# Kernel optimization log

Measured on AMD Instinct MI355X. Metric: run time of the kernel, lower is better.

Reference implementation:

```python
import jax, jax.numpy as jnp
import numpy as np

G, B, T, D, U = 3, 32, 1024, 512, 512  # branches, batch, time, feat dim, units

def setup_inputs() -> dict:
    key = jax.random.key(0)
    ks = jax.random.split(key, 8)
    s = 0.02
    return {
        "query": jax.random.normal(ks[0], (G, B, D), jnp.float32),
        "values": jax.random.normal(ks[1], (G, B, T, D), jnp.float32),
        "W1": jax.random.normal(ks[2], (G, D, U), jnp.float32) * s,
        "b1": jnp.zeros((G, U), jnp.float32),
        "W2": jax.random.normal(ks[3], (G, D, U), jnp.float32) * s,
        "b2": jnp.zeros((G, U), jnp.float32),
        "V": jax.random.normal(ks[4], (G, U), jnp.float32) * s,
        "bV": jnp.zeros((G,), jnp.float32),
    }

def reference(query, values, W1, b1, W2, b2, V, bV):
    # query: [G,B,D], values: [G,B,T,D]; G=3 independent additive-attention branches.
    qp = jnp.einsum('gbd,gdu->gbu', query, W1) + b1[:, None, :]          # [G,B,U]
    vp = jnp.einsum('gbtd,gdu->gbtu', values, W2) + b2[:, None, None, :]  # [G,B,T,U]
    feat = jnp.tanh(qp[:, :, None, :] + vp)                               # [G,B,T,U]
    score = jnp.einsum('gbtu,gu->gbt', feat, V) + bV[:, None, None]       # [G,B,T]
    weights = jax.nn.softmax(score, axis=2)                               # softmax over time
    context = jnp.einsum('gbt,gbtd->gbd', weights, values)                # [G,B,D]
    return context, weights[..., None]  # matches tf.stack outputs: [3,B,D], [3,B,T,1]
```

## Files before the change

### kernel.cpp

```cpp
#include <hip/hip_runtime.h>
#include <cstdint>
#include <cstddef>

#define NG 3
#define NB 32
#define NT 1024
#define ND 512
#define NU 512

typedef __bf16 bf16x8 __attribute__((ext_vector_type(8)));
typedef float  f32x16 __attribute__((ext_vector_type(16)));

static __device__ __forceinline__ unsigned int f2bf(float f) {
    union { float f; unsigned int u; } v; v.f = f;
    return (v.u + 0x7FFFu + ((v.u >> 16) & 1u)) >> 16;
}

static __device__ __forceinline__ bf16x8 ld_bf16x8(const char* base, int off) {
    return __builtin_bit_cast(bf16x8, *(const uint4*)(base + off));
}

__global__ __launch_bounds__(256) void prep_qb_kernel(
    const float* __restrict__ query, const float* __restrict__ W1,
    const float* __restrict__ b1, const float* __restrict__ b2,
    float* __restrict__ qb)
{
    __shared__ float qs[NB][ND];
    const int g  = blockIdx.x >> 3;
    const int uc = blockIdx.x & 7;
    const int tid = threadIdx.x;

    const float4* qsrc = (const float4*)(query + (size_t)g * NB * ND);
    #pragma unroll
    for (int i = 0; i < 16; ++i)
        ((float4*)&qs[0][0])[tid + i * 256] = qsrc[tid + i * 256];
    __syncthreads();

    const int u  = uc * 64 + (tid & 63);
    const int b0 = tid >> 6;
    float acc[8] = {};
    const float* w1col = W1 + (size_t)g * ND * NU + u;
    for (int d = 0; d < ND; ++d) {
        float w = w1col[(size_t)d * NU];
        #pragma unroll
        for (int j = 0; j < 8; ++j)
            acc[j] = fmaf(qs[b0 + 4 * j][d], w, acc[j]);
    }
    const float bias = b1[g * NU + u] + b2[g * NU + u];
    #pragma unroll
    for (int j = 0; j < 8; ++j)
        qb[((size_t)g * NB + (b0 + 4 * j)) * NU + u] = acc[j] + bias;
}

__global__ __launch_bounds__(256) void prep_w2t_kernel(
    const float* __restrict__ W2, char* __restrict__ w2t)
{
    __shared__ float tile[64][65];
    const int g  = blockIdx.x >> 6;
    const int tb = blockIdx.x & 63;
    const int d0 = (tb >> 3) * 64;
    const int u0 = (tb & 7) * 64;
    const int tx = threadIdx.x & 63;
    const int ty = threadIdx.x >> 6;

    const float* src = W2 + (size_t)g * ND * NU;
    #pragma unroll
    for (int k = 0; k < 16; ++k) {
        int r = ty + 4 * k;
        tile[r][tx] = src[(size_t)(d0 + r) * NU + (u0 + tx)];
    }
    __syncthreads();
    char* dstg = w2t + (size_t)g * 16 * 32768;
    #pragma unroll
    for (int k = 0; k < 16; ++k) {
        int ul = ty + 4 * k;
        int u  = u0 + ul;
        int d  = d0 + tx;
        unsigned short h = (unsigned short)f2bf(tile[tx][ul]);
        int r = u & 31;
        size_t off = (size_t)(u >> 5) * 32768
                   + (size_t)(((r << 10) | (d << 1)) ^ ((r & 7) << 4));
        *(unsigned short*)(dstg + off) = h;
    }
}

__global__ __launch_bounds__(256, 2) void score_kernel(
    const float* __restrict__ values, const char* __restrict__ w2t,
    const float* __restrict__ qb, const float* __restrict__ Vvec,
    const float* __restrict__ bV, float* __restrict__ scores)
{
    __shared__ char  Bs[2][32768];
    __shared__ float qbs[NU];
    __shared__ float Vs[NU];

    const int blk = blockIdx.x;
    const int g   = blk >> 8;
    const int rem = blk & 255;
    const int b   = rem >> 3;
    const int t0  = (rem & 7) << 7;
    const int tid  = threadIdx.x;
    const int lane = tid & 63;
    const int wave = tid >> 6;

    const char* w2g = w2t + ((size_t)g << 19);

    {
        const char* src = w2g + (wave << 13) + (lane << 4);
        char* dst = &Bs[0][wave << 13];
        #pragma unroll
        for (int i = 0; i < 8; ++i)
            __builtin_amdgcn_global_load_lds(
                (const __attribute__((address_space(1))) void*)(src + (i << 10)),
                (__attribute__((address_space(3))) void*)(dst + (i << 10)),
                16, 0, 0);
    }

    bf16x8 afrag[32];
    {
        const int arow_t = t0 + (wave << 5) + (lane & 31);
        const float* arow = values + (((size_t)g * NB + b) * NT + arow_t) * ND;
        const int acol = (lane >> 5) << 3;
        #pragma unroll
        for (int kk = 0; kk < 32; ++kk) {
            const float4* ap = (const float4*)(arow + (kk << 4) + acol);
            float4 v0 = ap[0], v1 = ap[1];
            union { bf16x8 v; unsigned int u[4]; } t;
            t.u[0] = f2bf(v0.x) | (f2bf(v0.y) << 16);
            t.u[1] = f2bf(v0.z) | (f2bf(v0.w) << 16);
            t.u[2] = f2bf(v1.x) | (f2bf(v1.y) << 16);
            t.u[3] = f2bf(v1.z) | (f2bf(v1.w) << 16);
            afrag[kk] = t.v;
        }
    }

    {
        const float* qsrc = qb + ((size_t)g * NB + b) * NU;
        qbs[tid]       = qsrc[tid];
        qbs[tid + 256] = qsrc[tid + 256];
        Vs[tid]        = Vvec[g * NU + tid];
        Vs[tid + 256]  = Vvec[g * NU + tid + 256];
    }

    asm volatile("s_waitcnt vmcnt(0) lgkmcnt(0)" ::: "memory");
    __builtin_amdgcn_s_barrier();

    const int brow  = lane & 31;
    const int bbase = (brow << 10) + ((lane >> 5) << 4);
    const int bswz  = (lane & 7) << 4;

    float p[16] = {};

    #pragma unroll 1
    for (int uc = 0; uc < 16; ++uc) {
        if (uc < 15) {
            const char* src = w2g + (((size_t)(uc + 1)) << 15) + (wave << 13) + (lane << 4);
            char* dst = &Bs[(uc + 1) & 1][wave << 13];
            #pragma unroll
            for (int i = 0; i < 8; ++i)
                __builtin_amdgcn_global_load_lds(
                    (const __attribute__((address_space(1))) void*)(src + (i << 10)),
                    (__attribute__((address_space(3))) void*)(dst + (i << 10)),
                    16, 0, 0);
        }

        const char* bsL = Bs[uc & 1];
        f32x16 acc = (f32x16)(0.0f);
        #pragma unroll
        for (int kk = 0; kk < 32; ++kk) {
            bf16x8 bfv = ld_bf16x8(bsL, (bbase + (kk << 5)) ^ bswz);
            acc = __builtin_amdgcn_mfma_f32_32x32x16_bf16(afrag[kk], bfv, acc, 0, 0, 0);
        }

        const int u = (uc << 5) + brow;
        const float qv = qbs[u], vv = Vs[u];
        #pragma unroll
        for (int r = 0; r < 16; ++r) {
            float x  = acc[r] + qv;
            float e  = __expf(-2.f * fabsf(x));
            float th = (1.f - e) / (1.f + e);
            th = copysignf(th, x);
            p[r] = fmaf(th, vv, p[r]);
        }

        asm volatile("s_waitcnt vmcnt(0)" ::: "memory");
        __builtin_amdgcn_s_barrier();
    }

    #pragma unroll
    for (int r = 0; r < 16; ++r) {
        float v = p[r];
        v += __shfl_xor(v, 1);
        v += __shfl_xor(v, 2);
        v += __shfl_xor(v, 4);
        v += __shfl_xor(v, 8);
        v += __shfl_xor(v, 16);
        p[r] = v;
    }
    if ((lane & 31) == 0) {
        const float bv = bV[g];
        float* srow = scores + ((size_t)g * NB + b) * NT + t0 + (wave << 5);
        #pragma unroll
        for (int r = 0; r < 16; ++r) {
            int t_local = (r & 3) + 8 * (r >> 2) + 4 * (lane >> 5);
            srow[t_local] = p[r] + bv;
        }
    }
}

__global__ __launch_bounds__(256) void finish_kernel(
    const float* __restrict__ scores, const float* __restrict__ values,
    float* __restrict__ out_ctx, float* __restrict__ out_w)
{
    __shared__ float sl[NT];
    __shared__ float red[16];
    const int gb  = blockIdx.x;
    const int tid = threadIdx.x;
    const int lane = tid & 63, wid = tid >> 6;

    const float* srow = scores + (size_t)gb * NT;
    float s[4];
    #pragma unroll
    for (int j = 0; j < 4; ++j) s[j] = srow[tid + 256 * j];

    float m = fmaxf(fmaxf(s[0], s[1]), fmaxf(s[2], s[3]));
    #pragma unroll
    for (int mask = 32; mask; mask >>= 1) m = fmaxf(m, __shfl_xor(m, mask));
    if (lane == 0) red[wid] = m;
    __syncthreads();
    const float gm = fmaxf(fmaxf(red[0], red[1]), fmaxf(red[2], red[3]));

    float e[4], ps = 0.f;
    #pragma unroll
    for (int j = 0; j < 4; ++j) { e[j] = __expf(s[j] - gm); ps += e[j]; }
    #pragma unroll
    for (int mask = 32; mask; mask >>= 1) ps += __shfl_xor(ps, mask);
    if (lane == 0) red[8 + wid] = ps;
    __syncthreads();
    const float inv = 1.f / (red[8] + red[9] + red[10] + red[11]);

    #pragma unroll
    for (int j = 0; j < 4; ++j) {
        float w = e[j] * inv;
        sl[tid + 256 * j] = w;
        out_w[(size_t)gb * NT + tid + 256 * j] = w;
    }
    __syncthreads();

    const float* vbase = values + (size_t)gb * NT * ND + 2 * tid;
    float2 a0 = {0.f, 0.f}, a1 = {0.f, 0.f}, a2 = {0.f, 0.f}, a3 = {0.f, 0.f};
    #pragma unroll 2
    for (int t = 0; t < NT; t += 4) {
        float2 v0 = *(const float2*)(vbase + (size_t)(t + 0) * ND);
        float2 v1 = *(const float2*)(vbase + (size_t)(t + 1) * ND);
        float2 v2 = *(const float2*)(vbase + (size_t)(t + 2) * ND);
        float2 v3 = *(const float2*)(vbase + (size_t)(t + 3) * ND);
        float w0 = sl[t], w1 = sl[t + 1], w2 = sl[t + 2], w3 = sl[t + 3];
        a0.x = fmaf(w0, v0.x, a0.x); a0.y = fmaf(w0, v0.y, a0.y);
        a1.x = fmaf(w1, v1.x, a1.x); a1.y = fmaf(w1, v1.y, a1.y);
        a2.x = fmaf(w2, v2.x, a2.x); a2.y = fmaf(w2, v2.y, a2.y);
        a3.x = fmaf(w3, v3.x, a3.x); a3.y = fmaf(w3, v3.y, a3.y);
    }
    float2 r;
    r.x = (a0.x + a1.x) + (a2.x + a3.x);
    r.y = (a0.y + a1.y) + (a2.y + a3.y);
    *(float2*)(out_ctx + (size_t)gb * ND + 2 * tid) = r;
}

extern "C" void kernel_launch(void* const* d_in, const int* in_sizes, int n_in,
                              void* d_out, int out_size, void* d_ws, size_t ws_size,
                              hipStream_t stream)
{
    (void)in_sizes; (void)n_in; (void)out_size; (void)ws_size;
    const float* query  = (const float*)d_in[0];
    const float* values = (const float*)d_in[1];
    const float* W1     = (const float*)d_in[2];
    const float* b1     = (const float*)d_in[3];
    const float* W2     = (const float*)d_in[4];
    const float* b2     = (const float*)d_in[5];
    const float* Vv     = (const float*)d_in[6];
    const float* bV     = (const float*)d_in[7];

    float* out_ctx = (float*)d_out;
    float* out_w   = out_ctx + (size_t)NG * NB * ND;

    float* qb     = (float*)d_ws;
    float* scores = qb + (size_t)NG * NB * NU;
    char*  w2t    = (char*)(scores + (size_t)NG * NB * NT);

    prep_qb_kernel <<<NG * 8,             256, 0, stream>>>(query, W1, b1, b2, qb);
    prep_w2t_kernel<<<NG * 64,            256, 0, stream>>>(W2, w2t);
    score_kernel   <<<NG * NB * (NT/128), 256, 0, stream>>>(values, w2t, qb, Vv, bV, scores);
    finish_kernel  <<<NG * NB,            256, 0, stream>>>(scores, values, out_ctx, out_w);
}
```

Baseline: 181.5 us.

## Triple-buffer W2 in half-K stages and split finish kernel across D slices

```diff
diff --git a/kernel.cpp b/kernel.cpp
--- a/kernel.cpp
+++ b/kernel.cpp
@@ -84,12 +84,12 @@
     }
 }
 
-__global__ __launch_bounds__(256, 2) void score_kernel(
+__global__ __launch_bounds__(256, 3) void score_kernel(
     const float* __restrict__ values, const char* __restrict__ w2t,
     const float* __restrict__ qb, const float* __restrict__ Vvec,
     const float* __restrict__ bV, float* __restrict__ scores)
 {
-    __shared__ char  Bs[2][32768];
+    __shared__ char  Bs[3][16384];
     __shared__ float qbs[NU];
     __shared__ float Vs[NU];
 
@@ -104,16 +104,20 @@
 
     const char* w2g = w2t + ((size_t)g << 19);
 
-    {
-        const char* src = w2g + (wave << 13) + (lane << 4);
-        char* dst = &Bs[0][wave << 13];
-        #pragma unroll
-        for (int i = 0; i < 8; ++i)
+    auto stage = [&](int ph) {
+        const char* src = w2g + ((size_t)(ph >> 1) << 15) + ((ph & 1) << 9)
+                        + (wave << 13) + ((lane >> 5) << 10) + ((lane & 31) << 4);
+        char* dst = &Bs[ph % 3][(wave << 12) + (lane << 4)];
+        #pragma unroll
+        for (int i = 0; i < 4; ++i)
             __builtin_amdgcn_global_load_lds(
-                (const __attribute__((address_space(1))) void*)(src + (i << 10)),
+                (const __attribute__((address_space(1))) void*)(src + (i << 11)),
                 (__attribute__((address_space(3))) void*)(dst + (i << 10)),
                 16, 0, 0);
-    }
+    };
+
+    stage(0);
+    stage(1);
 
     bf16x8 afrag[32];
     {
@@ -141,49 +145,52 @@
         Vs[tid + 256]  = Vvec[g * NU + tid + 256];
     }
 
-    asm volatile("s_waitcnt vmcnt(0) lgkmcnt(0)" ::: "memory");
+    asm volatile("s_waitcnt vmcnt(4) lgkmcnt(0)" ::: "memory");
     __builtin_amdgcn_s_barrier();
 
     const int brow  = lane & 31;
-    const int bbase = (brow << 10) + ((lane >> 5) << 4);
-    const int bswz  = (lane & 7) << 4;
+    const int bswz  = (brow & 7) << 4;
+    const int bbase = (brow << 9) + ((lane >> 5) << 4);
 
     float p[16] = {};
+    f32x16 acc = (f32x16)(0.0f);
 
     #pragma unroll 1
-    for (int uc = 0; uc < 16; ++uc) {
-        if (uc < 15) {
-            const char* src = w2g + (((size_t)(uc + 1)) << 15) + (wave << 13) + (lane << 4);
-            char* dst = &Bs[(uc + 1) & 1][wave << 13];
+    for (int ph = 0; ph < 32; ++ph) {
+        if (ph < 30) stage(ph + 2);
+
+        const char* bsL = Bs[ph % 3];
+        if ((ph & 1) == 0) acc = (f32x16)(0.0f);
+
+        __builtin_amdgcn_s_setprio(1);
+        #pragma unroll
+        for (int kk = 0; kk < 16; ++kk) {
+            bf16x8 bfv = ld_bf16x8(bsL, (bbase + (kk << 5)) ^ bswz);
+            acc = __builtin_amdgcn_mfma_f32_32x32x16_bf16(
+                      afrag[((ph & 1) << 4) + kk], bfv, acc, 0, 0, 0);
+        }
+        __builtin_amdgcn_s_setprio(0);
+
+        if (ph & 1) {
+            const int u = ((ph >> 1) << 5) + brow;
+            const float qv = qbs[u], vv = Vs[u];
             #pragma unroll
-            for (int i = 0; i < 8; ++i)
-                __builtin_amdgcn_global_load_lds(
-                    (const __attribute__((address_space(1))) void*)(src + (i << 10)),
-                    (__attribute__((address_space(3))) void*)(dst + (i << 10)),
-                    16, 0, 0);
-        }
-
-        const char* bsL = Bs[uc & 1];
-        f32x16 acc = (f32x16)(0.0f);
-        #pragma unroll
-        for (int kk = 0; kk < 32; ++kk) {
-            bf16x8 bfv = ld_bf16x8(bsL, (bbase + (kk << 5)) ^ bswz);
-            acc = __builtin_amdgcn_mfma_f32_32x32x16_bf16(afrag[kk], bfv, acc, 0, 0, 0);
-        }
-
-        const int u = (uc << 5) + brow;
-        const float qv = qbs[u], vv = Vs[u];
-        #pragma unroll
-        for (int r = 0; r < 16; ++r) {
-            float x  = acc[r] + qv;
-            float e  = __expf(-2.f * fabsf(x));
-            float th = (1.f - e) / (1.f + e);
-            th = copysignf(th, x);
-            p[r] = fmaf(th, vv, p[r]);
-        }
-
-        asm volatile("s_waitcnt vmcnt(0)" ::: "memory");
-        __builtin_amdgcn_s_barrier();
+            for (int r = 0; r < 16; ++r) {
+                float x  = acc[r] + qv;
+                float e  = __expf(-2.f * fabsf(x));
+                float th = (1.f - e) / (1.f + e);
+                th = copysignf(th, x);
+                p[r] = fmaf(th, vv, p[r]);
+            }
+        }
+
+        if (ph < 30) {
+            asm volatile("s_waitcnt vmcnt(4)" ::: "memory");
+            __builtin_amdgcn_s_barrier();
+        } else if (ph == 30) {
+            asm volatile("s_waitcnt vmcnt(0)" ::: "memory");
+            __builtin_amdgcn_s_barrier();
+        }
     }
 
     #pragma unroll
@@ -213,7 +220,10 @@
 {
     __shared__ float sl[NT];
     __shared__ float red[16];
-    const int gb  = blockIdx.x;
+    __shared__ float cred[4][128];
+    const int blk   = blockIdx.x;
+    const int gb    = blk >> 2;
+    const int slice = blk & 3;
     const int tid = threadIdx.x;
     const int lane = tid & 63, wid = tid >> 6;
 
@@ -242,28 +252,28 @@
     for (int j = 0; j < 4; ++j) {
         float w = e[j] * inv;
         sl[tid + 256 * j] = w;
-        out_w[(size_t)gb * NT + tid + 256 * j] = w;
-    }
-    __syncthreads();
-
-    const float* vbase = values + (size_t)gb * NT * ND + 2 * tid;
-    float2 a0 = {0.f, 0.f}, a1 = {0.f, 0.f}, a2 = {0.f, 0.f}, a3 = {0.f, 0.f};
-    #pragma unroll 2
-    for (int t = 0; t < NT; t += 4) {
-        float2 v0 = *(const float2*)(vbase + (size_t)(t + 0) * ND);
-        float2 v1 = *(const float2*)(vbase + (size_t)(t + 1) * ND);
-        float2 v2 = *(const float2*)(vbase + (size_t)(t + 2) * ND);
-        float2 v3 = *(const float2*)(vbase + (size_t)(t + 3) * ND);
-        float w0 = sl[t], w1 = sl[t + 1], w2 = sl[t + 2], w3 = sl[t + 3];
-        a0.x = fmaf(w0, v0.x, a0.x); a0.y = fmaf(w0, v0.y, a0.y);
-        a1.x = fmaf(w1, v1.x, a1.x); a1.y = fmaf(w1, v1.y, a1.y);
-        a2.x = fmaf(w2, v2.x, a2.x); a2.y = fmaf(w2, v2.y, a2.y);
-        a3.x = fmaf(w3, v3.x, a3.x); a3.y = fmaf(w3, v3.y, a3.y);
-    }
-    float2 r;
-    r.x = (a0.x + a1.x) + (a2.x + a3.x);
-    r.y = (a0.y + a1.y) + (a2.y + a3.y);
-    *(float2*)(out_ctx + (size_t)gb * ND + 2 * tid) = r;
+        if (slice == 0) out_w[(size_t)gb * NT + tid + 256 * j] = w;
+    }
+    __syncthreads();
+
+    const int dp = tid & 63;
+    const int tg = tid >> 6;
+    const float* vbase = values + (size_t)gb * NT * ND + slice * 128 + dp * 2;
+    float ax = 0.f, ay = 0.f;
+    #pragma unroll 4
+    for (int t = tg; t < NT; t += 4) {
+        float2 v = *(const float2*)(vbase + (size_t)t * ND);
+        float w = sl[t];
+        ax = fmaf(w, v.x, ax);
+        ay = fmaf(w, v.y, ay);
+    }
+    cred[tg][dp * 2]     = ax;
+    cred[tg][dp * 2 + 1] = ay;
+    __syncthreads();
+    if (tid < 128) {
+        float r = cred[0][tid] + cred[1][tid] + cred[2][tid] + cred[3][tid];
+        out_ctx[(size_t)gb * ND + slice * 128 + tid] = r;
+    }
 }
 
 extern "C" void kernel_launch(void* const* d_in, const int* in_sizes, int n_in,
@@ -290,5 +300,5 @@
     prep_qb_kernel <<<NG * 8,             256, 0, stream>>>(query, W1, b1, b2, qb);
     prep_w2t_kernel<<<NG * 64,            256, 0, stream>>>(W2, w2t);
     score_kernel   <<<NG * NB * (NT/128), 256, 0, stream>>>(values, w2t, qb, Vv, bV, scores);
-    finish_kernel  <<<NG * NB,            256, 0, stream>>>(scores, values, out_ctx, out_w);
-}
+    finish_kernel  <<<NG * NB * 4,        256, 0, stream>>>(scores, values, out_ctx, out_w);
+}
```

After: 361.2 us. 1.99x slower.
